# Kernel tuning notes

Measured on AMD Instinct MI355X. Metric: run time of the kernel, lower is better.

Reference implementation:

```python
import jax, jax.numpy as jnp
import numpy as np

B, T, D = 2, 2048, 1024
H, DH = 16, 64
WINDOW = 256
SCALE = DH ** -0.5


def setup_inputs() -> dict:
    key = jax.random.key(0)
    ks = jax.random.split(key, 5)
    x = jax.random.normal(ks[0], (B, T, D), dtype=jnp.float32)
    # Linear params (y = x @ W + b form)
    w_qkv = jax.random.normal(ks[1], (D, 3 * D), dtype=jnp.float32) * (D ** -0.5)
    b_qkv = jnp.zeros((3 * D,), dtype=jnp.float32)
    w_out = jax.random.normal(ks[2], (D, D), dtype=jnp.float32) * (D ** -0.5)
    b_out = jnp.zeros((D,), dtype=jnp.float32)
    return {"x": x, "w_qkv": w_qkv, "b_qkv": b_qkv, "w_out": w_out, "b_out": b_out}


def reference(x, w_qkv, b_qkv, w_out, b_out):
    Bs, Ts, Ds = x.shape
    qkv = x @ w_qkv + b_qkv  # [B,T,3D]
    q, k, v = jnp.split(qkv, 3, axis=-1)
    # [B,H,T,dh]
    def heads(t):
        return t.reshape(Bs, Ts, H, DH).transpose(0, 2, 1, 3)
    q, k, v = heads(q), heads(k), heads(v)
    scores = jnp.einsum('bhqd,bhkd->bhqk', q, k) * SCALE
    i = jnp.arange(Ts)[:, None]
    j = jnp.arange(Ts)[None, :]
    # allowed: i - WINDOW <= j <= i  (causal + local window)
    allowed = (j <= i) & (j >= i - WINDOW)
    scores = jnp.where(allowed, scores, -jnp.inf)
    attn = jax.nn.softmax(scores, axis=-1)  # dropout is identity in eval
    out = jnp.einsum('bhqk,bhkd->bhqd', attn, v)
    out = out.transpose(0, 2, 1, 3).reshape(Bs, Ts, Ds)
    return out @ w_out + b_out
```

## Files before the change

kernel.cpp:

```cpp
#include <hip/hip_runtime.h>

#define BN 2
#define T_DIM 2048
#define D_DIM 1024
#define H_N 16
#define DH_N 64
#define WIN 256
#define NROWS (BN * T_DIM)
#define KDIM 1024

typedef __attribute__((ext_vector_type(8))) short bf16x8;
typedef __attribute__((ext_vector_type(4))) float f32x4;
typedef __attribute__((ext_vector_type(8))) unsigned short ushort8;
typedef __attribute__((ext_vector_type(4))) unsigned short u16x4;

static __device__ __forceinline__ unsigned short f2bf(float f) {
  unsigned int u = __float_as_uint(f);
  unsigned int r = (u + 0x7FFFu + ((u >> 16) & 1u)) >> 16;
  return (unsigned short)r;
}

static __device__ __forceinline__ void gl_lds16(const void* g, void* l) {
  __builtin_amdgcn_global_load_lds(
      (const __attribute__((address_space(1))) unsigned int*)g,
      (__attribute__((address_space(3))) unsigned int*)l, 16, 0, 0);
}

__global__ __launch_bounds__(256) void convert_bf(const float* __restrict__ src,
                                                  unsigned short* __restrict__ dst) {
  int i = (blockIdx.x * 256 + threadIdx.x) * 8;
  float4 a = *(const float4*)(src + i);
  float4 b = *(const float4*)(src + i + 4);
  ushort8 o;
  o[0] = f2bf(a.x); o[1] = f2bf(a.y); o[2] = f2bf(a.z); o[3] = f2bf(a.w);
  o[4] = f2bf(b.x); o[5] = f2bf(b.y); o[6] = f2bf(b.z); o[7] = f2bf(b.w);
  *(ushort8*)(dst + i) = o;
}

__global__ __launch_bounds__(256) void convert_t(const float* __restrict__ src,
                                                 unsigned short* __restrict__ dst,
                                                 int R, int C) {
  __shared__ float tile[64][65];
  const int t = threadIdx.x;
  const int bc = blockIdx.x * 64, br = blockIdx.y * 64;
#pragma unroll
  for (int i = 0; i < 16; ++i) {
    int idx = i * 256 + t;
    int r = idx >> 6, c = idx & 63;
    tile[r][c] = src[(size_t)(br + r) * C + bc + c];
  }
  __syncthreads();
#pragma unroll
  for (int i = 0; i < 16; ++i) {
    int idx = i * 256 + t;
    int r = idx >> 6, c = idx & 63;
    dst[(size_t)(bc + r) * R + br + c] = f2bf(tile[c][r]);
  }
}

__global__ __launch_bounds__(512) void gemm_qkv_p4(
    const unsigned short* __restrict__ A, const unsigned short* __restrict__ Bt,
    const float* __restrict__ bias, unsigned short* __restrict__ qo,
    unsigned short* __restrict__ ko, unsigned short* __restrict__ vto) {
  __shared__ unsigned short As[4][8192];
  __shared__ unsigned short Bs[4][6144];

  const int tid = threadIdx.x;
  const int w = tid >> 6, l = tid & 63;
  const int wr = w >> 2, wc = w & 3;
  const bool wlt4 = (w < 4);
  const int l15 = l & 15, kslc = l >> 4;

  const int id = blockIdx.x;
  const int wg = (id & 7) * 32 + (id >> 3);
  const int bx = wg & 15, by = wg >> 4;
  const int r0 = by * 256, c0 = bx * 192;

  const unsigned short* Ag = A + (size_t)r0 * KDIM;
  const unsigned short* Bg = Bt + (size_t)c0 * KDIM;

  f32x4 acc[8][3];
#pragma unroll
  for (int i = 0; i < 8; ++i)
#pragma unroll
    for (int j = 0; j < 3; ++j) acc[i][j] = (f32x4){0.f, 0.f, 0.f, 0.f};

  const int srow = l >> 2;
  const int srcslot = (l & 3) ^ ((l >> 3) & 3);

#define STAGE_Q(T, BUF)                                                        \
  do {                                                                         \
    const size_t kk0 = (size_t)(T) * 32;                                       \
    gl_lds16(Ag + (size_t)(w * 16 + srow) * KDIM + kk0 + srcslot * 8,          \
             (char*)&As[BUF][0] + w * 1024);                                   \
    gl_lds16(Ag + (size_t)(128 + w * 16 + srow) * KDIM + kk0 + srcslot * 8,    \
             (char*)&As[BUF][0] + (8 + w) * 1024);                             \
    gl_lds16(Bg + (size_t)(w * 16 + srow) * KDIM + kk0 + srcslot * 8,          \
             (char*)&Bs[BUF][0] + w * 1024);                                   \
    if (wlt4)                                                                  \
      gl_lds16(Bg + (size_t)(128 + w * 16 + srow) * KDIM + kk0 + srcslot * 8,  \
               (char*)&Bs[BUF][0] + (8 + w) * 1024);                           \
  } while (0)

#define QCOMPUTE(CB)                                                           \
  do {                                                                         \
    bf16x8 af[4], bfr[3];                                                      \
    _Pragma("unroll") for (int mi = 0; mi < 4; ++mi) {                         \
      int row = wr * 128 + mi * 16 + l15;                                      \
      af[mi] = *(const bf16x8*)((const char*)&As[CB][0] + row * 64 +           \
                                ((kslc ^ ((row >> 1) & 3)) << 4));             \
    }                                                                          \
    _Pragma("unroll") for (int ni = 0; ni < 3; ++ni) {                         \
      int row = wc * 48 + ni * 16 + l15;                                       \
      bfr[ni] = *(const bf16x8*)((const char*)&Bs[CB][0] + row * 64 +          \
                                 ((kslc ^ ((row >> 1) & 3)) << 4));            \
    }                                                                          \
    __builtin_amdgcn_s_setprio(1);                                             \
    _Pragma("unroll") for (int mi = 0; mi < 4; ++mi)                           \
        _Pragma("unroll") for (int ni = 0; ni < 3; ++ni) acc[mi][ni] =         \
            __builtin_amdgcn_mfma_f32_16x16x32_bf16(af[mi], bfr[ni],           \
                                                    acc[mi][ni], 0, 0, 0);     \
    __builtin_amdgcn_s_setprio(0);                                             \
    _Pragma("unroll") for (int mi = 0; mi < 4; ++mi) {                         \
      int row = wr * 128 + (mi + 4) * 16 + l15;                                \
      af[mi] = *(const bf16x8*)((const char*)&As[CB][0] + row * 64 +           \
                                ((kslc ^ ((row >> 1) & 3)) << 4));             \
    }                                                                          \
    __builtin_amdgcn_s_setprio(1);                                             \
    _Pragma("unroll") for (int mi = 0; mi < 4; ++mi)                           \
        _Pragma("unroll") for (int ni = 0; ni < 3; ++ni) acc[mi + 4][ni] =     \
            __builtin_amdgcn_mfma_f32_16x16x32_bf16(af[mi], bfr[ni],           \
                                                    acc[mi + 4][ni], 0, 0, 0); \
    __builtin_amdgcn_s_setprio(0);                                             \
  } while (0)

  STAGE_Q(0, 0);
  STAGE_Q(1, 1);

  for (int t = 0; t < 30; ++t) {
    STAGE_Q(t + 2, (t + 2) & 3);
    if (wlt4) asm volatile("s_waitcnt vmcnt(8)" ::: "memory");
    else      asm volatile("s_waitcnt vmcnt(6)" ::: "memory");
    __builtin_amdgcn_s_barrier();
    QCOMPUTE(t & 3);
  }
  if (wlt4) asm volatile("s_waitcnt vmcnt(4)" ::: "memory");
  else      asm volatile("s_waitcnt vmcnt(3)" ::: "memory");
  __builtin_amdgcn_s_barrier();
  QCOMPUTE(2);
  asm volatile("s_waitcnt vmcnt(0)" ::: "memory");
  __builtin_amdgcn_s_barrier();
  QCOMPUTE(3);
#undef STAGE_Q
#undef QCOMPUTE

#pragma unroll
  for (int ni = 0; ni < 3; ++ni) {
    const int col0 = c0 + wc * 48 + ni * 16;
    const int which = col0 >> 10;
    const int h = (col0 >> 6) & 15;
    const int dh = (col0 & 63) + l15;
    const float bv = bias[col0 + l15];
#pragma unroll
    for (int mi = 0; mi < 8; ++mi) {
      int row = r0 + wr * 128 + mi * 16 + (l >> 4) * 4;
      int b_ = row >> 11, t0 = row & 2047;
      if (which == 2) {
        u16x4 pk;
#pragma unroll
        for (int j = 0; j < 4; ++j) pk[j] = f2bf(acc[mi][ni][j] + bv);
        *(u16x4*)(vto + ((size_t)(b_ * H_N + h) * DH_N + dh) * T_DIM + t0) = pk;
      } else {
        float mul = (which == 0) ? 0.125f : 1.0f;
        unsigned short* dst = (which == 0) ? qo : ko;
#pragma unroll
        for (int j = 0; j < 4; ++j)
          dst[((size_t)(b_ * H_N + h) * T_DIM + t0 + j) * DH_N + dh] =
              f2bf((acc[mi][ni][j] + bv) * mul);
      }
    }
  }
}

__global__ __launch_bounds__(256) void gemm_out_p4(
    const unsigned short* __restrict__ A, const unsigned short* __restrict__ Bt,
    const float* __restrict__ bias, float* __restrict__ fo) {
  __shared__ unsigned short As[4][4096];
  __shared__ unsigned short Bs[4][4096];

  const int tid = threadIdx.x;
  const int w = tid >> 6, l = tid & 63;
  const int wr = w >> 1, wc = w & 1;
  const int l15 = l & 15, kslc = l >> 4;

  const int id = blockIdx.x;
  const int wg = (id & 7) * 32 + (id >> 3);
  const int bx = wg & 7, by = wg >> 3;
  const int r0 = by * 128, c0 = bx * 128;

  const unsigned short* Ag = A + (size_t)r0 * KDIM;
  const unsigned short* Bg = Bt + (size_t)c0 * KDIM;

  f32x4 acc[4][4];
#pragma unroll
  for (int i = 0; i < 4; ++i)
#pragma unroll
    for (int j = 0; j < 4; ++j) acc[i][j] = (f32x4){0.f, 0.f, 0.f, 0.f};

  const int srow = l >> 2;
  const int srcslot = (l & 3) ^ ((l >> 3) & 3);

#define STAGE_O(T, BUF)                                                        \
  do {                                                                         \
    const size_t kk0 = (size_t)(T) * 32;                                       \
    gl_lds16(Ag + (size_t)(w * 16 + srow) * KDIM + kk0 + srcslot * 8,          \
             (char*)&As[BUF][0] + w * 1024);                                   \
    gl_lds16(Ag + (size_t)(64 + w * 16 + srow) * KDIM + kk0 + srcslot * 8,     \
             (char*)&As[BUF][0] + (4 + w) * 1024);                             \
    gl_lds16(Bg + (size_t)(w * 16 + srow) * KDIM + kk0 + srcslot * 8,          \
             (char*)&Bs[BUF][0] + w * 1024);                                   \
    gl_lds16(Bg + (size_t)(64 + w * 16 + srow) * KDIM + kk0 + srcslot * 8,     \
             (char*)&Bs[BUF][0] + (4 + w) * 1024);                             \
  } while (0)

#define OCOMPUTE(CB)                                                           \
  do {                                                                         \
    bf16x8 af[4], bfr[4];                                                      \
    _Pragma("unroll") for (int mi = 0; mi < 4; ++mi) {                         \
      int row = wr * 64 + mi * 16 + l15;                                       \
      af[mi] = *(const bf16x8*)((const char*)&As[CB][0] + row * 64 +           \
                                ((kslc ^ ((row >> 1) & 3)) << 4));             \
    }                                                                          \
    _Pragma("unroll") for (int ni = 0; ni < 4; ++ni) {                         \
      int row = wc * 64 + ni * 16 + l15;                                       \
      bfr[ni] = *(const bf16x8*)((const char*)&Bs[CB][0] + row * 64 +          \
                                 ((kslc ^ ((row >> 1) & 3)) << 4));            \
    }                                                                          \
    __builtin_amdgcn_s_setprio(1);                                             \
    _Pragma("unroll") for (int mi = 0; mi < 4; ++mi)                           \
        _Pragma("unroll") for (int ni = 0; ni < 4; ++ni) acc[mi][ni] =         \
            __builtin_amdgcn_mfma_f32_16x16x32_bf16(af[mi], bfr[ni],           \
                                                    acc[mi][ni], 0, 0, 0);     \
    __builtin_amdgcn_s_setprio(0);                                             \
  } while (0)

  STAGE_O(0, 0);
  STAGE_O(1, 1);

  for (int t = 0; t < 30; ++t) {
    STAGE_O(t + 2, (t + 2) & 3);
    asm volatile("s_waitcnt vmcnt(8)" ::: "memory");
    __builtin_amdgcn_s_barrier();
    OCOMPUTE(t & 3);
  }
  asm volatile("s_waitcnt vmcnt(4)" ::: "memory");
  __builtin_amdgcn_s_barrier();
  OCOMPUTE(2);
  asm volatile("s_waitcnt vmcnt(0)" ::: "memory");
  __builtin_amdgcn_s_barrier();
  OCOMPUTE(3);
#undef STAGE_O
#undef OCOMPUTE

#pragma unroll
  for (int mi = 0; mi < 4; ++mi) {
#pragma unroll
    for (int ni = 0; ni < 4; ++ni) {
      int row = r0 + wr * 64 + mi * 16 + (l >> 4) * 4;
      int col = c0 + wc * 64 + ni * 16 + l15;
      float bv = bias[col];
#pragma unroll
      for (int j = 0; j < 4; ++j)
        fo[(size_t)(row + j) * D_DIM + col] = acc[mi][ni][j] + bv;
    }
  }
}

__global__ __launch_bounds__(256) void attn_mfma(
    const unsigned short* __restrict__ qbf,
    const unsigned short* __restrict__ kbf,
    const unsigned short* __restrict__ vtbf,
    unsigned short* __restrict__ ctx) {
  __shared__ unsigned short Ks[64 * 64];
  __shared__ unsigned short Vs[64 * 64];
  const int tid = threadIdx.x;
  const int w = tid >> 6, l = tid & 63;
  const int g = l >> 4, ln = l & 15;
  const int qt = blockIdx.x & 31;
  const int bh = blockIdx.x >> 5;
  const int q0 = qt * 64;
  const int q_abs = q0 + w * 16 + ln;

  const unsigned short* kp = kbf + (size_t)bh * T_DIM * DH_N;
  const unsigned short* vtp = vtbf + (size_t)bh * DH_N * T_DIM;

  bf16x8 qf0, qf1;
  {
    const unsigned short* qp = qbf + ((size_t)bh * T_DIM + q_abs) * DH_N;
    qf0 = *(const bf16x8*)(qp + g * 8);
    qf1 = *(const bf16x8*)(qp + 32 + g * 8);
  }

  f32x4 acc_o[4];
#pragma unroll
  for (int nd = 0; nd < 4; ++nd) acc_o[nd] = (f32x4){0.f, 0.f, 0.f, 0.f};
  float m = -1e30f, lsum = 0.f;

  const int kt_lo = (q0 >= WIN) ? (q0 - WIN) : 0;
  for (int kt = kt_lo; kt <= q0; kt += 64) {
    __syncthreads();
#pragma unroll
    for (int i = 0; i < 2; ++i) {
      int chunk = i * 256 + tid;
      int row = chunk >> 3, c16 = chunk & 7;
      int sc16 = c16 ^ (row & 7);
      int kap = 32 * ((row >> 4) & 1) + 8 * ((row & 15) >> 2) + 4 * (row >> 5) +
                (row & 3);
      gl_lds16(kp + (size_t)(kt + kap) * DH_N + sc16 * 8, (char*)Ks + chunk * 16);
      gl_lds16(vtp + (size_t)row * T_DIM + kt + sc16 * 8, (char*)Vs + chunk * 16);
    }
    __syncthreads();

    f32x4 sacc[4];
#pragma unroll
    for (int nk = 0; nk < 4; ++nk) sacc[nk] = (f32x4){0.f, 0.f, 0.f, 0.f};
#pragma unroll
    for (int ks = 0; ks < 2; ++ks) {
      bf16x8 qf = ks ? qf1 : qf0;
#pragma unroll
      for (int nk = 0; nk < 4; ++nk) {
        int rrow = nk * 16 + ln;
        int c16 = ks * 4 + g;
        bf16x8 kf = *(const bf16x8*)((const char*)Ks + rrow * 128 +
                                     ((c16 ^ (rrow & 7)) * 16));
        sacc[nk] = __builtin_amdgcn_mfma_f32_16x16x32_bf16(kf, qf, sacc[nk], 0, 0, 0);
      }
    }

    float p[4][4];
    float tm = -1e30f;
#pragma unroll
    for (int nk = 0; nk < 4; ++nk)
#pragma unroll
      for (int j = 0; j < 4; ++j) {
        int k_abs = kt + 32 * (nk & 1) + 8 * g + 4 * (nk >> 1) + j;
        float s = sacc[nk][j];
        bool ok = (k_abs <= q_abs) && (k_abs + WIN >= q_abs);
        s = ok ? s : -1e30f;
        p[nk][j] = s;
        tm = fmaxf(tm, s);
      }
    tm = fmaxf(tm, __shfl_xor(tm, 16, 64));
    tm = fmaxf(tm, __shfl_xor(tm, 32, 64));
    float mn = fmaxf(m, tm);
    float sc = __expf(m - mn);
    float ps = 0.f;
#pragma unroll
    for (int nk = 0; nk < 4; ++nk)
#pragma unroll
      for (int j = 0; j < 4; ++j) {
        p[nk][j] = __expf(p[nk][j] - mn);
        ps += p[nk][j];
      }
    ps += __shfl_xor(ps, 16, 64);
    ps += __shfl_xor(ps, 32, 64);
    lsum = lsum * sc + ps;
    m = mn;
#pragma unroll
    for (int nd = 0; nd < 4; ++nd) {
      acc_o[nd][0] *= sc; acc_o[nd][1] *= sc;
      acc_o[nd][2] *= sc; acc_o[nd][3] *= sc;
    }

    unsigned int pk[4][2];
#pragma unroll
    for (int nk = 0; nk < 4; ++nk) {
      pk[nk][0] = (unsigned)f2bf(p[nk][0]) | ((unsigned)f2bf(p[nk][1]) << 16);
      pk[nk][1] = (unsigned)f2bf(p[nk][2]) | ((unsigned)f2bf(p[nk][3]) << 16);
    }

#pragma unroll
    for (int ks = 0; ks < 2; ++ks) {
      union { unsigned int d[4]; bf16x8 v; } pf;
      pf.d[0] = pk[ks][0];     pf.d[1] = pk[ks][1];
      pf.d[2] = pk[2 + ks][0]; pf.d[3] = pk[2 + ks][1];
#pragma unroll
      for (int nd = 0; nd < 4; ++nd) {
        int drow = nd * 16 + ln;
        int c16 = ks * 4 + g;
        bf16x8 vf = *(const bf16x8*)((const char*)Vs + drow * 128 +
                                     ((c16 ^ (drow & 7)) * 16));
        acc_o[nd] = __builtin_amdgcn_mfma_f32_16x16x32_bf16(vf, pf.v, acc_o[nd],
                                                            0, 0, 0);
      }
    }
  }

  float inv = 1.f / lsum;
  const int b_ = bh >> 4, h = bh & 15;
  unsigned short* op = ctx + ((size_t)b_ * T_DIM + q_abs) * D_DIM + h * DH_N;
#pragma unroll
  for (int nd = 0; nd < 4; ++nd) {
    u16x4 o;
#pragma unroll
    for (int j = 0; j < 4; ++j) o[j] = f2bf(acc_o[nd][j] * inv);
    *(u16x4*)(op + nd * 16 + g * 4) = o;
  }
}

extern "C" void kernel_launch(void* const* d_in, const int* in_sizes, int n_in,
                              void* d_out, int out_size, void* d_ws,
                              size_t ws_size, hipStream_t stream) {
  const float* x = (const float*)d_in[0];
  const float* w_qkv = (const float*)d_in[1];
  const float* b_qkv = (const float*)d_in[2];
  const float* w_out = (const float*)d_in[3];
  const float* b_out = (const float*)d_in[4];
  float* out = (float*)d_out;

  const size_t per = (size_t)BN * H_N * T_DIM * DH_N;
  unsigned short* qbf = (unsigned short*)d_ws;
  unsigned short* kbf = qbf + per;
  unsigned short* vtbf = kbf + per;
  unsigned short* xbf = vtbf + per;
  unsigned short* wqkvt = xbf + (size_t)NROWS * D_DIM;
  unsigned short* woutt = wqkvt + (size_t)3 * D_DIM * D_DIM;
  unsigned short* ctxbf = woutt + (size_t)D_DIM * D_DIM;

  convert_bf<<<dim3(NROWS * D_DIM / (256 * 8)), dim3(256), 0, stream>>>(x, xbf);
  convert_t<<<dim3(3 * D_DIM / 64, D_DIM / 64), dim3(256), 0, stream>>>(
      w_qkv, wqkvt, D_DIM, 3 * D_DIM);
  convert_t<<<dim3(D_DIM / 64, D_DIM / 64), dim3(256), 0, stream>>>(
      w_out, woutt, D_DIM, D_DIM);

  gemm_qkv_p4<<<dim3(256), dim3(512), 0, stream>>>(xbf, wqkvt, b_qkv, qbf, kbf,
                                                   vtbf);

  attn_mfma<<<dim3(BN * H_N * (T_DIM / 64)), dim3(256), 0, stream>>>(
      qbf, kbf, vtbf, ctxbf);

  gemm_out_p4<<<dim3(256), dim3(256), 0, stream>>>(ctxbf, woutt, b_out, out);
}
```

Baseline: 90.10 us.

## Restructure QKV GEMM into double-buffered K=64 tiles with interleaved staging

The QKV projection GEMM moves from a 4-stage ring of 32-wide K tiles to a 2-stage double buffer of 64-wide K tiles. Loads for the next tile are spread across four compute phases, and barriers are placed between them, in the style of an 8-wave ping-pong schedule. LDS rows are 128 bytes with an XOR swizzle on the 16-byte chunk index. The aim is better overlap of global-to-LDS loads with MFMA clusters and fewer loop iterations, at the cost of many extra barriers per iteration and shallower prefetch. A shared MFMA macro is also introduced elsewhere as a refactor.

```diff
diff --git a/kernel.cpp b/kernel.cpp
--- a/kernel.cpp
+++ b/kernel.cpp
@@ -25,6 +25,8 @@
       (const __attribute__((address_space(1))) unsigned int*)g,
       (__attribute__((address_space(3))) unsigned int*)l, 16, 0, 0);
 }
+
+#define MFMA16(a, b, c) __builtin_amdgcn_mfma_f32_16x16x32_bf16(a, b, c, 0, 0, 0)
 
 __global__ __launch_bounds__(256) void convert_bf(const float* __restrict__ src,
                                                   unsigned short* __restrict__ dst) {
@@ -58,17 +60,16 @@
   }
 }
 
-__global__ __launch_bounds__(512) void gemm_qkv_p4(
+__global__ __launch_bounds__(512) void gemm_qkv_8p(
     const unsigned short* __restrict__ A, const unsigned short* __restrict__ Bt,
     const float* __restrict__ bias, unsigned short* __restrict__ qo,
     unsigned short* __restrict__ ko, unsigned short* __restrict__ vto) {
-  __shared__ unsigned short As[4][8192];
-  __shared__ unsigned short Bs[4][6144];
+  __shared__ unsigned short As[2][256 * 64];
+  __shared__ unsigned short Bs[2][192 * 64];
 
   const int tid = threadIdx.x;
   const int w = tid >> 6, l = tid & 63;
   const int wr = w >> 2, wc = w & 3;
-  const bool wlt4 = (w < 4);
   const int l15 = l & 15, kslc = l >> 4;
 
   const int id = blockIdx.x;
@@ -85,74 +86,102 @@
 #pragma unroll
     for (int j = 0; j < 3; ++j) acc[i][j] = (f32x4){0.f, 0.f, 0.f, 0.f};
 
-  const int srow = l >> 2;
-  const int srcslot = (l & 3) ^ ((l >> 3) & 3);
-
-#define STAGE_Q(T, BUF)                                                        \
+  const int grow = tid >> 3;
+  const int gcol = (tid & 7) ^ (grow & 7);
+
+#define STAGE_A(T, BUF, CH)                                                    \
+  gl_lds16(Ag + (size_t)((CH)*64 + grow) * KDIM + (T)*64 + gcol * 8,           \
+           (char*)&As[BUF][0] + (CH)*8192 + w * 1024)
+#define STAGE_B(T, BUF, CH)                                                    \
+  gl_lds16(Bg + (size_t)((CH)*64 + grow) * KDIM + (T)*64 + gcol * 8,           \
+           (char*)&Bs[BUF][0] + (CH)*8192 + w * 1024)
+
+#define LDA(CB, mi, ks)                                                        \
+  (*(const bf16x8*)((const char*)&As[CB][0] +                                  \
+                    (wr * 128 + (mi)*16 + l15) * 128 +                         \
+                    ((((ks)*4 + kslc) ^ (l15 & 7)) << 4)))
+#define LDB(CB, ni, ks)                                                        \
+  (*(const bf16x8*)((const char*)&Bs[CB][0] +                                  \
+                    (wc * 48 + (ni)*16 + l15) * 128 +                          \
+                    ((((ks)*4 + kslc) ^ (l15 & 7)) << 4)))
+
+#define CLUSTER12(B_, A0, A1, A2, A3, B0, B1, B2)                              \
   do {                                                                         \
-    const size_t kk0 = (size_t)(T) * 32;                                       \
-    gl_lds16(Ag + (size_t)(w * 16 + srow) * KDIM + kk0 + srcslot * 8,          \
-             (char*)&As[BUF][0] + w * 1024);                                   \
-    gl_lds16(Ag + (size_t)(128 + w * 16 + srow) * KDIM + kk0 + srcslot * 8,    \
-             (char*)&As[BUF][0] + (8 + w) * 1024);                             \
-    gl_lds16(Bg + (size_t)(w * 16 + srow) * KDIM + kk0 + srcslot * 8,          \
-             (char*)&Bs[BUF][0] + w * 1024);                                   \
-    if (wlt4)                                                                  \
-      gl_lds16(Bg + (size_t)(128 + w * 16 + srow) * KDIM + kk0 + srcslot * 8,  \
-               (char*)&Bs[BUF][0] + (8 + w) * 1024);                           \
-  } while (0)
-
-#define QCOMPUTE(CB)                                                           \
-  do {                                                                         \
-    bf16x8 af[4], bfr[3];                                                      \
-    _Pragma("unroll") for (int mi = 0; mi < 4; ++mi) {                         \
-      int row = wr * 128 + mi * 16 + l15;                                      \
-      af[mi] = *(const bf16x8*)((const char*)&As[CB][0] + row * 64 +           \
-                                ((kslc ^ ((row >> 1) & 3)) << 4));             \
-    }                                                                          \
-    _Pragma("unroll") for (int ni = 0; ni < 3; ++ni) {                         \
-      int row = wc * 48 + ni * 16 + l15;                                       \
-      bfr[ni] = *(const bf16x8*)((const char*)&Bs[CB][0] + row * 64 +          \
-                                 ((kslc ^ ((row >> 1) & 3)) << 4));            \
-    }                                                                          \
     __builtin_amdgcn_s_setprio(1);                                             \
-    _Pragma("unroll") for (int mi = 0; mi < 4; ++mi)                           \
-        _Pragma("unroll") for (int ni = 0; ni < 3; ++ni) acc[mi][ni] =         \
-            __builtin_amdgcn_mfma_f32_16x16x32_bf16(af[mi], bfr[ni],           \
-                                                    acc[mi][ni], 0, 0, 0);     \
-    __builtin_amdgcn_s_setprio(0);                                             \
-    _Pragma("unroll") for (int mi = 0; mi < 4; ++mi) {                         \
-      int row = wr * 128 + (mi + 4) * 16 + l15;                                \
-      af[mi] = *(const bf16x8*)((const char*)&As[CB][0] + row * 64 +           \
-                                ((kslc ^ ((row >> 1) & 3)) << 4));             \
-    }                                                                          \
-    __builtin_amdgcn_s_setprio(1);                                             \
-    _Pragma("unroll") for (int mi = 0; mi < 4; ++mi)                           \
-        _Pragma("unroll") for (int ni = 0; ni < 3; ++ni) acc[mi + 4][ni] =     \
-            __builtin_amdgcn_mfma_f32_16x16x32_bf16(af[mi], bfr[ni],           \
-                                                    acc[mi + 4][ni], 0, 0, 0); \
+    acc[B_ + 0][0] = MFMA16(A0, B0, acc[B_ + 0][0]);                           \
+    acc[B_ + 0][1] = MFMA16(A0, B1, acc[B_ + 0][1]);                           \
+    acc[B_ + 0][2] = MFMA16(A0, B2, acc[B_ + 0][2]);                           \
+    acc[B_ + 1][0] = MFMA16(A1, B0, acc[B_ + 1][0]);                           \
+    acc[B_ + 1][1] = MFMA16(A1, B1, acc[B_ + 1][1]);                           \
+    acc[B_ + 1][2] = MFMA16(A1, B2, acc[B_ + 1][2]);                           \
+    acc[B_ + 2][0] = MFMA16(A2, B0, acc[B_ + 2][0]);                           \
+    acc[B_ + 2][1] = MFMA16(A2, B1, acc[B_ + 2][1]);                           \
+    acc[B_ + 2][2] = MFMA16(A2, B2, acc[B_ + 2][2]);                           \
+    acc[B_ + 3][0] = MFMA16(A3, B0, acc[B_ + 3][0]);                           \
+    acc[B_ + 3][1] = MFMA16(A3, B1, acc[B_ + 3][1]);                           \
+    acc[B_ + 3][2] = MFMA16(A3, B2, acc[B_ + 3][2]);                           \
     __builtin_amdgcn_s_setprio(0);                                             \
   } while (0)
 
-  STAGE_Q(0, 0);
-  STAGE_Q(1, 1);
-
-  for (int t = 0; t < 30; ++t) {
-    STAGE_Q(t + 2, (t + 2) & 3);
-    if (wlt4) asm volatile("s_waitcnt vmcnt(8)" ::: "memory");
-    else      asm volatile("s_waitcnt vmcnt(6)" ::: "memory");
+  STAGE_A(0, 0, 0); STAGE_A(0, 0, 1); STAGE_A(0, 0, 2); STAGE_A(0, 0, 3);
+  STAGE_B(0, 0, 0); STAGE_B(0, 0, 1); STAGE_B(0, 0, 2);
+
+#pragma unroll 1
+  for (int t = 0; t < 15; ++t) {
+    const int cb = t & 1, nb = cb ^ 1;
+    STAGE_A(t + 1, nb, 0); STAGE_A(t + 1, nb, 1);
+    asm volatile("s_waitcnt vmcnt(2)" ::: "memory");
     __builtin_amdgcn_s_barrier();
-    QCOMPUTE(t & 3);
-  }
-  if (wlt4) asm volatile("s_waitcnt vmcnt(4)" ::: "memory");
-  else      asm volatile("s_waitcnt vmcnt(3)" ::: "memory");
-  __builtin_amdgcn_s_barrier();
-  QCOMPUTE(2);
+    {
+      bf16x8 a0 = LDA(cb, 0, 0), a1 = LDA(cb, 1, 0), a2 = LDA(cb, 2, 0),
+             a3 = LDA(cb, 3, 0);
+      bf16x8 b0 = LDB(cb, 0, 0), b1 = LDB(cb, 1, 0), b2 = LDB(cb, 2, 0);
+      CLUSTER12(0, a0, a1, a2, a3, b0, b1, b2);
+      __builtin_amdgcn_s_barrier();
+      bf16x8 a4 = LDA(cb, 4, 0), a5 = LDA(cb, 5, 0), a6 = LDA(cb, 6, 0),
+             a7 = LDA(cb, 7, 0);
+      STAGE_A(t + 1, nb, 2); STAGE_A(t + 1, nb, 3);
+      __builtin_amdgcn_s_barrier();
+      CLUSTER12(4, a4, a5, a6, a7, b0, b1, b2);
+      __builtin_amdgcn_s_barrier();
+      bf16x8 c0_ = LDA(cb, 0, 1), c1_ = LDA(cb, 1, 1), c2_ = LDA(cb, 2, 1),
+             c3_ = LDA(cb, 3, 1);
+      bf16x8 d0 = LDB(cb, 0, 1), d1 = LDB(cb, 1, 1), d2 = LDB(cb, 2, 1);
+      STAGE_B(t + 1, nb, 0); STAGE_B(t + 1, nb, 1);
+      __builtin_amdgcn_s_barrier();
+      CLUSTER12(0, c0_, c1_, c2_, c3_, d0, d1, d2);
+      __builtin_amdgcn_s_barrier();
+      bf16x8 c4 = LDA(cb, 4, 1), c5 = LDA(cb, 5, 1), c6 = LDA(cb, 6, 1),
+             c7 = LDA(cb, 7, 1);
+      STAGE_B(t + 1, nb, 2);
+      __builtin_amdgcn_s_barrier();
+      CLUSTER12(4, c4, c5, c6, c7, d0, d1, d2);
+      __builtin_amdgcn_s_barrier();
+    }
+  }
   asm volatile("s_waitcnt vmcnt(0)" ::: "memory");
   __builtin_amdgcn_s_barrier();
-  QCOMPUTE(3);
-#undef STAGE_Q
-#undef QCOMPUTE
+  {
+    bf16x8 a0 = LDA(1, 0, 0), a1 = LDA(1, 1, 0), a2 = LDA(1, 2, 0),
+           a3 = LDA(1, 3, 0);
+    bf16x8 b0 = LDB(1, 0, 0), b1 = LDB(1, 1, 0), b2 = LDB(1, 2, 0);
+    CLUSTER12(0, a0, a1, a2, a3, b0, b1, b2);
+    bf16x8 a4 = LDA(1, 4, 0), a5 = LDA(1, 5, 0), a6 = LDA(1, 6, 0),
+           a7 = LDA(1, 7, 0);
+    CLUSTER12(4, a4, a5, a6, a7, b0, b1, b2);
+    bf16x8 c0_ = LDA(1, 0, 1), c1_ = LDA(1, 1, 1), c2_ = LDA(1, 2, 1),
+           c3_ = LDA(1, 3, 1);
+    bf16x8 d0 = LDB(1, 0, 1), d1 = LDB(1, 1, 1), d2 = LDB(1, 2, 1);
+    CLUSTER12(0, c0_, c1_, c2_, c3_, d0, d1, d2);
+    bf16x8 c4 = LDA(1, 4, 1), c5 = LDA(1, 5, 1), c6 = LDA(1, 6, 1),
+           c7 = LDA(1, 7, 1);
+    CLUSTER12(4, c4, c5, c6, c7, d0, d1, d2);
+  }
+#undef STAGE_A
+#undef STAGE_B
+#undef LDA
+#undef LDB
+#undef CLUSTER12
 
 #pragma unroll
   for (int ni = 0; ni < 3; ++ni) {
@@ -239,8 +268,7 @@
     __builtin_amdgcn_s_setprio(1);                                             \
     _Pragma("unroll") for (int mi = 0; mi < 4; ++mi)                           \
         _Pragma("unroll") for (int ni = 0; ni < 4; ++ni) acc[mi][ni] =         \
-            __builtin_amdgcn_mfma_f32_16x16x32_bf16(af[mi], bfr[ni],           \
-                                                    acc[mi][ni], 0, 0, 0);     \
+            MFMA16(af[mi], bfr[ni], acc[mi][ni]);                              \
     __builtin_amdgcn_s_setprio(0);                                             \
   } while (0)
 
@@ -333,7 +361,7 @@
         int c16 = ks * 4 + g;
         bf16x8 kf = *(const bf16x8*)((const char*)Ks + rrow * 128 +
                                      ((c16 ^ (rrow & 7)) * 16));
-        sacc[nk] = __builtin_amdgcn_mfma_f32_16x16x32_bf16(kf, qf, sacc[nk], 0, 0, 0);
+        sacc[nk] = MFMA16(kf, qf, sacc[nk]);
       }
     }
 
@@ -390,8 +418,7 @@
         int c16 = ks * 4 + g;
         bf16x8 vf = *(const bf16x8*)((const char*)Vs + drow * 128 +
                                      ((c16 ^ (drow & 7)) * 16));
-        acc_o[nd] = __builtin_amdgcn_mfma_f32_16x16x32_bf16(vf, pf.v, acc_o[nd],
-                                                            0, 0, 0);
+        acc_o[nd] = MFMA16(vf, pf.v, acc_o[nd]);
       }
     }
   }
@@ -433,7 +460,7 @@
   convert_t<<<dim3(D_DIM / 64, D_DIM / 64), dim3(256), 0, stream>>>(
       w_out, woutt, D_DIM, D_DIM);
 
-  gemm_qkv_p4<<<dim3(256), dim3(512), 0, stream>>>(xbf, wqkvt, b_qkv, qbf, kbf,
+  gemm_qkv_8p<<<dim3(256), dim3(512), 0, stream>>>(xbf, wqkvt, b_qkv, qbf, kbf,
                                                    vtbf);
 
   attn_mfma<<<dim3(BN * H_N * (T_DIM / 64)), dim3(256), 0, stream>>>(
```

Measured after the change: 92.40 us. 1.03x slower.
